# Optimization experiments

Hardware: AMD Instinct MI355X
Metric: run time of the kernel (lower is better)

Reference implementation:

```python
import jax, jax.numpy as jnp
import numpy as np
from jax import lax

COS_BASIS_NO = 24
SCALE = 6.0
SHIFT = 1.0


def make_kern_basis(T_no):
    # [24, T_no] raised-cosine log-time basis, matching the torch loop exactly
    i = jnp.arange(COS_BASIS_NO, dtype=jnp.float32)
    phi = (jnp.pi / 2.0) * i                                  # [24]
    x = jnp.arange(T_no, dtype=jnp.float32)
    raw = SCALE * jnp.log(x + SHIFT + 1e-7)                   # [T_no]
    basis = 0.5 * jnp.cos(raw[None, :] - phi[:, None]) + 0.5  # [24, T_no]
    inside = (raw[None, :] >= phi[:, None] - jnp.pi) & (raw[None, :] <= phi[:, None] + jnp.pi)
    return jnp.where(inside, basis, 0.0)


def causal_grouped_conv(x, kern, sub_no, T_no):
    # x: [B, sub_no, T], kern: [sub_no*hid, T_no] (already flipped like torch)
    # left-pad T_no-1 zeros == the torch zero-padded buffer; cross-correlation
    rhs = kern[:, None, :]  # OIH with I=1 per group
    return lax.conv_general_dilated(
        x, rhs, window_strides=(1,), padding=[(T_no - 1, 0)],
        feature_group_count=sub_no,
        dimension_numbers=("NCH", "OIH", "NCH"))


def setup_inputs() -> dict:
    key = jax.random.key(0)
    ks = jax.random.split(key, 10)
    B, T_data = 8, 5000
    sub_no, E_no, I_no, T_no, hid_no = 20, 2000, 200, 400, 16
    inp = {
        "S_e": jax.random.uniform(ks[0], (B, T_data, E_no), dtype=jnp.float32),
        "S_i": jax.random.uniform(ks[1], (B, T_data, I_no), dtype=jnp.float32),
        "E_scale": jnp.zeros((E_no,), jnp.float32),
        "I_scale": jnp.zeros((I_no,), jnp.float32),
        "W_e_layer1": jax.random.normal(ks[2], (sub_no * hid_no, COS_BASIS_NO), jnp.float32) * 0.01,
        "W_i_layer1": jax.random.normal(ks[3], (sub_no * hid_no, COS_BASIS_NO), jnp.float32) * 0.01,
        "W_layer2": jnp.full((sub_no, hid_no), -1.0, jnp.float32),
        "b_layer1": jnp.zeros((sub_no * hid_no,), jnp.float32),
        "C_syn_e_raw": jax.random.normal(ks[4], (sub_no, E_no), jnp.float32) * 0.01,
        "C_syn_i_raw": jax.random.normal(ks[5], (sub_no, I_no), jnp.float32) * 0.01,
        "V_o": jnp.zeros((1,), jnp.float32),
        "temp": jnp.asarray(1.0, jnp.float32),
        "T_no": T_no,
        "test": 1,
    }
    return inp


def reference(S_e, S_i, E_scale, I_scale, W_e_layer1, W_i_layer1, W_layer2,
              b_layer1, C_syn_e_raw, C_syn_i_raw, V_o, temp, T_no, test):
    sub_no = C_syn_e_raw.shape[0]
    hid_no = W_layer2.shape[1]
    B, T_data, _ = S_e.shape

    if test:
        C_syn_e = jax.nn.softmax(C_syn_e_raw / temp, axis=0)
        C_syn_i = jax.nn.softmax(C_syn_i_raw / temp, axis=0)
    else:
        eps = 1e-8
        ku, kv = jax.random.split(jax.random.key(42))
        u_e = jax.random.uniform(ku, C_syn_e_raw.shape, dtype=C_syn_e_raw.dtype)
        u_i = jax.random.uniform(kv, C_syn_i_raw.shape, dtype=C_syn_i_raw.dtype)
        g_e = -jnp.log(-jnp.log(u_e + eps) + eps)
        g_i = -jnp.log(-jnp.log(u_i + eps) + eps)
        C_syn_e = jax.nn.softmax((C_syn_e_raw + g_e) / temp, axis=0)
        C_syn_i = jax.nn.softmax((C_syn_i_raw + g_i) / temp, axis=0)

    # scale synapses and project onto subunits: [B,T,E] x [E,sub] -> [B,T,sub]
    syn_e = jnp.einsum("bte,se->bts", S_e * jnp.exp(E_scale)[None, None, :], C_syn_e)
    syn_i = jnp.einsum("bti,si->bts", S_i * jnp.exp(I_scale)[None, None, :], C_syn_i)

    kern_basis = make_kern_basis(T_no)                        # [24, T_no]
    ke = jnp.flip(W_e_layer1 @ kern_basis, axis=1)            # [sub*hid, T_no]
    ki = jnp.flip(W_i_layer1 @ kern_basis, axis=1)

    xe = jnp.transpose(syn_e, (0, 2, 1))                      # [B, sub, T]
    xi = jnp.transpose(syn_i, (0, 2, 1))
    conv_e = causal_grouped_conv(xe, ke, sub_no, T_no)        # [B, sub*hid, T]
    conv_i = causal_grouped_conv(xi, ki, sub_no, T_no)
    layer1 = jnp.tanh(conv_e + conv_i + b_layer1[None, :, None])

    # grouped 1x1 conv == per-subunit weighted reduction over hid
    h = layer1.reshape(B, sub_no, hid_no, T_data)
    sub_out = jnp.einsum("bshT,sh->bTs", h, jnp.exp(W_layer2))  # [B, T, sub]
    final = jnp.sum(sub_out, axis=-1) + V_o                    # [B, T]
    return final, sub_out, C_syn_e, C_syn_i
```

## Files before the change

kernel.cpp:

```cpp
#include <hip/hip_runtime.h>
#include <math.h>

#define PI_F 3.14159265358979323846f
#define BSTRIDE 404

__global__ __launch_bounds__(256) void prep_kernel(
    const float* __restrict__ Ce_raw, const float* __restrict__ Ci_raw,
    const float* __restrict__ Escale, const float* __restrict__ Iscale,
    const float* __restrict__ temp,
    float* __restrict__ CsT_e, float* __restrict__ CsT_i,
    float* __restrict__ basis,
    float* __restrict__ outCe, float* __restrict__ outCi)
{
    int id = blockIdx.x * 256 + threadIdx.x;
    if (id < 2000) {
        int e = id;
        float t = temp[0];
        float v[20];
        float m = -1e30f;
        #pragma unroll
        for (int s = 0; s < 20; ++s) { v[s] = Ce_raw[s * 2000 + e] / t; m = fmaxf(m, v[s]); }
        float sum = 0.f;
        #pragma unroll
        for (int s = 0; s < 20; ++s) { v[s] = expf(v[s] - m); sum += v[s]; }
        float inv = 1.f / sum;
        float sc = expf(Escale[e]);
        #pragma unroll
        for (int s = 0; s < 20; ++s) {
            float p = v[s] * inv;
            outCe[s * 2000 + e] = p;
            CsT_e[e * 20 + s] = p * sc;
        }
    } else if (id < 2200) {
        int e = id - 2000;
        float t = temp[0];
        float v[20];
        float m = -1e30f;
        #pragma unroll
        for (int s = 0; s < 20; ++s) { v[s] = Ci_raw[s * 200 + e] / t; m = fmaxf(m, v[s]); }
        float sum = 0.f;
        #pragma unroll
        for (int s = 0; s < 20; ++s) { v[s] = expf(v[s] - m); sum += v[s]; }
        float inv = 1.f / sum;
        float sc = expf(Iscale[e]);
        #pragma unroll
        for (int s = 0; s < 20; ++s) {
            float p = v[s] * inv;
            outCi[s * 200 + e] = p;
            CsT_i[e * 20 + s] = p * sc;
        }
    } else if (id < 2200 + 24 * BSTRIDE) {
        int idx = id - 2200;
        int j = idx / BSTRIDE, d = idx - j * BSTRIDE;
        float val = 0.f;
        if (d < 400) {
            float raw = 6.0f * logf((float)d + 1.0f + 1e-7f);
            float ph = (PI_F * 0.5f) * (float)j;
            if (raw >= ph - PI_F && raw <= ph + PI_F) val = 0.5f * cosf(raw - ph) + 0.5f;
        }
        basis[idx] = val;
    } else if (id < 11896 + 48) {
        int row = 2000 + (id - 11896);
        #pragma unroll
        for (int s = 0; s < 20; ++s) CsT_e[row * 20 + s] = 0.f;
    } else if (id < 11944 + 56) {
        int row = 200 + (id - 11944);
        #pragma unroll
        for (int s = 0; s < 20; ++s) CsT_i[row * 20 + s] = 0.f;
    }
}

template <int NCHUNK>
__global__ __launch_bounds__(256) void syn_kernel(
    const float* __restrict__ S, const float* __restrict__ CsT,
    float* __restrict__ syn, int Eno)
{
    __shared__ float4 tile[64 * 33];
    float* red = reinterpret_cast<float*>(tile);
    const int tid = threadIdx.x;
    const int lane = tid & 63;
    const int w = __builtin_amdgcn_readfirstlane(tid >> 6);
    const int r0 = blockIdx.x * 64;

    float acc[20];
    #pragma unroll
    for (int s = 0; s < 20; ++s) acc[s] = 0.f;

    for (int ch = 0; ch < NCHUNK; ++ch) {
        const int ebase = ch * 128;
        #pragma unroll
        for (int i = 0; i < 8; ++i) {
            int f = tid + i * 256;
            int row = f >> 5, col4 = f & 31;
            int e0 = ebase + col4 * 4;
            float4 v = make_float4(0.f, 0.f, 0.f, 0.f);
            if (e0 + 4 <= Eno)
                v = *reinterpret_cast<const float4*>(S + (size_t)(r0 + row) * Eno + e0);
            tile[row * 33 + col4] = v;
        }
        __syncthreads();

        const float4* crow = reinterpret_cast<const float4*>(CsT + (size_t)(ebase + w * 32) * 20);
        #pragma unroll
        for (int c4 = 0; c4 < 8; ++c4) {
            float4 v = tile[lane * 33 + w * 8 + c4];
            const float4* ct = crow + c4 * 20;
            float vv[4] = {v.x, v.y, v.z, v.w};
            #pragma unroll
            for (int q = 0; q < 4; ++q) {
                float sv = vv[q];
                #pragma unroll
                for (int c5 = 0; c5 < 5; ++c5) {
                    float4 cc = ct[q * 5 + c5];
                    acc[c5 * 4 + 0] = fmaf(sv, cc.x, acc[c5 * 4 + 0]);
                    acc[c5 * 4 + 1] = fmaf(sv, cc.y, acc[c5 * 4 + 1]);
                    acc[c5 * 4 + 2] = fmaf(sv, cc.z, acc[c5 * 4 + 2]);
                    acc[c5 * 4 + 3] = fmaf(sv, cc.w, acc[c5 * 4 + 3]);
                }
            }
        }
        __syncthreads();
    }

    #pragma unroll
    for (int s = 0; s < 20; ++s) red[(w * 64 + lane) * 21 + s] = acc[s];
    __syncthreads();

    #pragma unroll
    for (int i = 0; i < 5; ++i) {
        int p = tid + i * 256;
        int row = p & 63, s = p >> 6;
        float a = red[(0 * 64 + row) * 21 + s] + red[(1 * 64 + row) * 21 + s]
                + red[(2 * 64 + row) * 21 + s] + red[(3 * 64 + row) * 21 + s];
        int r = r0 + row;
        int b = r / 5000, t = r - b * 5000;
        syn[((size_t)b * 20 + s) * 5000 + t] = a;
    }
}

__device__ const int CJ_LO[24] = {0,0,0,0,0,0,0,0,0,4,4,8,12,16,20,28,36,48,64,84,108,140,184,240};
__device__ const int CJ_NB[24] = {1,1,1,1,2,2,3,3,4,4,5,6,7,9,12,15,19,25,31,41,53,65,54,40};

__device__ __forceinline__ int phys4(int g) {
    return (g & ~15) | ((g >> 1) & 7) | ((g & 1) << 3);
}

__global__ __launch_bounds__(128) void conv_kernel(
    const float* __restrict__ syn_e, const float* __restrict__ syn_i,
    const float* __restrict__ basis,
    const float* __restrict__ W_e, const float* __restrict__ W_i,
    const float* __restrict__ b1, const float* __restrict__ W2,
    float* __restrict__ sub_out)
{
    __shared__ float4 win4[16 + 464];
    float4* wbase = win4 + 16;
    float2* win2 = reinterpret_cast<float2*>(wbase);
    const int tid = threadIdx.x;
    const int tile = blockIdx.x, s = blockIdx.y, bz = blockIdx.z;
    const int t0 = tile * 512;

    const float* se = syn_e + ((size_t)bz * 20 + s) * 5000;
    const float* si = syn_i + ((size_t)bz * 20 + s) * 5000;
    for (int l = tid; l < 920; l += 128) {
        int t = t0 - 404 + l;
        float ve = 0.f, vi = 0.f;
        if ((unsigned)t < 5000u) { ve = se[t]; vi = si[t]; }
        int g = l >> 1;
        win2[2 * phys4(g) + (l & 1)] = make_float2(ve, vi);
    }
    __syncthreads();

    float z[16][4];
    #pragma unroll
    for (int h = 0; h < 16; ++h) {
        float bv = b1[s * 16 + h];
        #pragma unroll
        for (int k = 0; k < 4; ++k) z[h][k] = bv;
    }

    const int base = 4 * tid + 400;

    for (int j = 0; j < 24; ++j) {
        const float4* bj4 = reinterpret_cast<const float4*>(basis + j * BSTRIDE);
        const int lo = CJ_LO[j];
        const int nb = CJ_NB[j];
        const int co = lo >> 2;
        float be0 = 0.f, be1 = 0.f, be2 = 0.f, be3 = 0.f;
        float bi0 = 0.f, bi1 = 0.f, bi2 = 0.f, bi3 = 0.f;

        auto body = [&](const float4& V0, const float4& V1,
                        const float4& V2, const float4& V3, const float4& c) {
            be0 = fmaf(c.x, V2.x, be0); bi0 = fmaf(c.x, V2.y, bi0);
            be1 = fmaf(c.x, V2.z, be1); bi1 = fmaf(c.x, V2.w, bi1);
            be2 = fmaf(c.x, V3.x, be2); bi2 = fmaf(c.x, V3.y, bi2);
            be3 = fmaf(c.x, V3.z, be3); bi3 = fmaf(c.x, V3.w, bi3);
            be0 = fmaf(c.y, V1.z, be0); bi0 = fmaf(c.y, V1.w, bi0);
            be1 = fmaf(c.y, V2.x, be1); bi1 = fmaf(c.y, V2.y, bi1);
            be2 = fmaf(c.y, V2.z, be2); bi2 = fmaf(c.y, V2.w, bi2);
            be3 = fmaf(c.y, V3.x, be3); bi3 = fmaf(c.y, V3.y, bi3);
            be0 = fmaf(c.z, V1.x, be0); bi0 = fmaf(c.z, V1.y, bi0);
            be1 = fmaf(c.z, V1.z, be1); bi1 = fmaf(c.z, V1.w, bi1);
            be2 = fmaf(c.z, V2.x, be2); bi2 = fmaf(c.z, V2.y, bi2);
            be3 = fmaf(c.z, V2.z, be3); bi3 = fmaf(c.z, V2.w, bi3);
            be0 = fmaf(c.w, V0.z, be0); bi0 = fmaf(c.w, V0.w, bi0);
            be1 = fmaf(c.w, V1.x, be1); bi1 = fmaf(c.w, V1.y, bi1);
            be2 = fmaf(c.w, V1.z, be2); bi2 = fmaf(c.w, V1.w, bi2);
            be3 = fmaf(c.w, V2.x, be3); bi3 = fmaf(c.w, V2.y, bi3);
        };

        const int g0 = (base - lo) >> 1;
        auto LP = [&](int n, float4& lo4, float4& hi4) {
            int p = phys4(g0 - 2 * n);
            lo4 = wbase[p]; hi4 = wbase[p + 8];
        };

        float4 A0, A1, B0, B1, C0, C1, D0, D1;
        float4 E0, E1, F0, F1, G0, G1, H0, H1;
        LP(-1, A0, A1); LP(0, B0, B1); LP(1, C0, C1); LP(2, D0, D1);
        float4 cB = bj4[co], cC = bj4[co + 1], cD = bj4[co + 2];

        int bb = 0;
        while (bb + 8 <= nb) {
            LP(bb + 3, E0, E1); float4 cE = bj4[co + bb + 3];
            body(B0, B1, A0, A1, cB);
            LP(bb + 4, F0, F1); float4 cF = bj4[co + bb + 4];
            body(C0, C1, B0, B1, cC);
            LP(bb + 5, G0, G1); float4 cG = bj4[co + bb + 5];
            body(D0, D1, C0, C1, cD);
            LP(bb + 6, H0, H1); float4 cH = bj4[co + bb + 6];
            body(E0, E1, D0, D1, cE);
            LP(bb + 7, A0, A1); float4 cI = bj4[co + bb + 7];
            body(F0, F1, E0, E1, cF);
            LP(bb + 8, B0, B1); cB = bj4[co + bb + 8];
            body(G0, G1, F0, F1, cG);
            LP(bb + 9, C0, C1); cC = bj4[co + bb + 9];
            body(H0, H1, G0, G1, cH);
            LP(bb + 10, D0, D1); cD = bj4[co + bb + 10];
            body(A0, A1, H0, H1, cI);
            bb += 8;
        }
        int r = nb - bb;
        if (r > 0) { body(B0, B1, A0, A1, cB);
          if (r > 1) { body(C0, C1, B0, B1, cC);
            if (r > 2) { body(D0, D1, C0, C1, cD);
              if (r > 3) { LP(bb + 3, E0, E1); float4 cE = bj4[co + bb + 3];
                body(E0, E1, D0, D1, cE);
                if (r > 4) { LP(bb + 4, F0, F1); float4 cF = bj4[co + bb + 4];
                  body(F0, F1, E0, E1, cF);
                  if (r > 5) { LP(bb + 5, G0, G1); float4 cG = bj4[co + bb + 5];
                    body(G0, G1, F0, F1, cG);
                    if (r > 6) { LP(bb + 6, H0, H1); float4 cH = bj4[co + bb + 6];
                      body(H0, H1, G0, G1, cH); } } } } } } }

        #pragma unroll
        for (int h = 0; h < 16; ++h) {
            float we = W_e[(s * 16 + h) * 24 + j];
            float wi = W_i[(s * 16 + h) * 24 + j];
            z[h][0] = fmaf(we, be0, fmaf(wi, bi0, z[h][0]));
            z[h][1] = fmaf(we, be1, fmaf(wi, bi1, z[h][1]));
            z[h][2] = fmaf(we, be2, fmaf(wi, bi2, z[h][2]));
            z[h][3] = fmaf(we, be3, fmaf(wi, bi3, z[h][3]));
        }
    }

    float w2v[16];
    #pragma unroll
    for (int h = 0; h < 16; ++h) w2v[h] = __expf(W2[s * 16 + h]);

    #pragma unroll
    for (int k = 0; k < 4; ++k) {
        int t = t0 + 4 * tid + k;
        if (t < 5000) {
            float acc = 0.f;
            #pragma unroll
            for (int h = 0; h < 16; ++h) {
                float e2 = __expf(2.0f * z[h][k]);
                float th = 1.0f - 2.0f / (e2 + 1.0f);
                acc = fmaf(w2v[h], th, acc);
            }
            sub_out[((size_t)bz * 5000 + t) * 20 + s] = acc;
        }
    }
}

__global__ __launch_bounds__(256) void final_kernel(
    const float* __restrict__ sub_out, const float* __restrict__ V_o,
    float* __restrict__ fin)
{
    int r = blockIdx.x * 256 + threadIdx.x;
    if (r < 40000) {
        const float* p = sub_out + (size_t)r * 20;
        float a = V_o[0];
        #pragma unroll
        for (int s = 0; s < 20; ++s) a += p[s];
        fin[r] = a;
    }
}

extern "C" void kernel_launch(void* const* d_in, const int* in_sizes, int n_in,
                              void* d_out, int out_size, void* d_ws, size_t ws_size,
                              hipStream_t stream)
{
    const float* S_e     = (const float*)d_in[0];
    const float* S_i     = (const float*)d_in[1];
    const float* E_scale = (const float*)d_in[2];
    const float* I_scale = (const float*)d_in[3];
    const float* W_e     = (const float*)d_in[4];
    const float* W_i     = (const float*)d_in[5];
    const float* W2      = (const float*)d_in[6];
    const float* b1      = (const float*)d_in[7];
    const float* Ce_raw  = (const float*)d_in[8];
    const float* Ci_raw  = (const float*)d_in[9];
    const float* V_o     = (const float*)d_in[10];
    const float* temp    = (const float*)d_in[11];

    float* out     = (float*)d_out;
    float* fin     = out;
    float* sub_out = out + 40000;
    float* outCe   = out + 840000;
    float* outCi   = out + 880000;

    float* ws    = (float*)d_ws;
    float* CsT_e = ws;
    float* CsT_i = ws + 40960;
    float* basis = ws + 46080;
    float* syn_e = ws + 55776;
    float* syn_i = ws + 855776;

    prep_kernel<<<47, 256, 0, stream>>>(Ce_raw, Ci_raw, E_scale, I_scale, temp,
                                        CsT_e, CsT_i, basis, outCe, outCi);
    syn_kernel<16><<<625, 256, 0, stream>>>(S_e, CsT_e, syn_e, 2000);
    syn_kernel<2><<<625, 256, 0, stream>>>(S_i, CsT_i, syn_i, 200);
    conv_kernel<<<dim3(10, 20, 8), 128, 0, stream>>>(syn_e, syn_i, basis,
                                                     W_e, W_i, b1, W2, sub_out);
    final_kernel<<<157, 256, 0, stream>>>(sub_out, V_o, fin);
}
```

Before: 310.7 us.

## Split syn projection over E into two halves and merge syn kernels

The excitatory projection is split into two K-halves (8 chunks each) run as separate grid slices, and the inhibitory projection joins them in one 3-slice launch. The goal is more blocks in flight across the CUs and one fewer kernel launch. The conv kernel adds the two partial results when it loads its window. The cost is an extra partial buffer in the workspace plus one more global read per conv window element. The S_i slice is much lighter than the others, so the load is uneven across blocks.

```diff
diff --git a/kernel.cpp b/kernel.cpp
--- a/kernel.cpp
+++ b/kernel.cpp
@@ -70,10 +70,11 @@
     }
 }
 
-template <int NCHUNK>
 __global__ __launch_bounds__(256) void syn_kernel(
-    const float* __restrict__ S, const float* __restrict__ CsT,
-    float* __restrict__ syn, int Eno)
+    const float* __restrict__ Se, const float* __restrict__ Si,
+    const float* __restrict__ Ce, const float* __restrict__ Ci,
+    float* __restrict__ outA, float* __restrict__ outB,
+    float* __restrict__ outI)
 {
     __shared__ float4 tile[64 * 33];
     float* red = reinterpret_cast<float*>(tile);
@@ -81,13 +82,21 @@
     const int lane = tid & 63;
     const int w = __builtin_amdgcn_readfirstlane(tid >> 6);
     const int r0 = blockIdx.x * 64;
+    const int z = blockIdx.z;
+
+    const float* S   = (z == 2) ? Si : Se;
+    const float* CsT = (z == 2) ? Ci : Ce;
+    float* out       = (z == 0) ? outA : (z == 1) ? outB : outI;
+    const int Eno    = (z == 2) ? 200 : 2000;
+    const int ch0    = (z == 1) ? 8 : 0;
+    const int nch    = (z == 2) ? 2 : 8;
 
     float acc[20];
     #pragma unroll
     for (int s = 0; s < 20; ++s) acc[s] = 0.f;
 
-    for (int ch = 0; ch < NCHUNK; ++ch) {
-        const int ebase = ch * 128;
+    for (int cc = 0; cc < nch; ++cc) {
+        const int ebase = (ch0 + cc) * 128;
         #pragma unroll
         for (int i = 0; i < 8; ++i) {
             int f = tid + i * 256;
@@ -111,11 +120,11 @@
                 float sv = vv[q];
                 #pragma unroll
                 for (int c5 = 0; c5 < 5; ++c5) {
-                    float4 cc = ct[q * 5 + c5];
-                    acc[c5 * 4 + 0] = fmaf(sv, cc.x, acc[c5 * 4 + 0]);
-                    acc[c5 * 4 + 1] = fmaf(sv, cc.y, acc[c5 * 4 + 1]);
-                    acc[c5 * 4 + 2] = fmaf(sv, cc.z, acc[c5 * 4 + 2]);
-                    acc[c5 * 4 + 3] = fmaf(sv, cc.w, acc[c5 * 4 + 3]);
+                    float4 cc2 = ct[q * 5 + c5];
+                    acc[c5 * 4 + 0] = fmaf(sv, cc2.x, acc[c5 * 4 + 0]);
+                    acc[c5 * 4 + 1] = fmaf(sv, cc2.y, acc[c5 * 4 + 1]);
+                    acc[c5 * 4 + 2] = fmaf(sv, cc2.z, acc[c5 * 4 + 2]);
+                    acc[c5 * 4 + 3] = fmaf(sv, cc2.w, acc[c5 * 4 + 3]);
                 }
             }
         }
@@ -134,7 +143,7 @@
                 + red[(2 * 64 + row) * 21 + s] + red[(3 * 64 + row) * 21 + s];
         int r = r0 + row;
         int b = r / 5000, t = r - b * 5000;
-        syn[((size_t)b * 20 + s) * 5000 + t] = a;
+        out[((size_t)b * 20 + s) * 5000 + t] = a;
     }
 }
 
@@ -146,8 +155,8 @@
 }
 
 __global__ __launch_bounds__(128) void conv_kernel(
-    const float* __restrict__ syn_e, const float* __restrict__ syn_i,
-    const float* __restrict__ basis,
+    const float* __restrict__ syn_eA, const float* __restrict__ syn_eB,
+    const float* __restrict__ syn_i, const float* __restrict__ basis,
     const float* __restrict__ W_e, const float* __restrict__ W_i,
     const float* __restrict__ b1, const float* __restrict__ W2,
     float* __restrict__ sub_out)
@@ -159,12 +168,13 @@
     const int tile = blockIdx.x, s = blockIdx.y, bz = blockIdx.z;
     const int t0 = tile * 512;
 
-    const float* se = syn_e + ((size_t)bz * 20 + s) * 5000;
-    const float* si = syn_i + ((size_t)bz * 20 + s) * 5000;
+    const float* seA = syn_eA + ((size_t)bz * 20 + s) * 5000;
+    const float* seB = syn_eB + ((size_t)bz * 20 + s) * 5000;
+    const float* si  = syn_i  + ((size_t)bz * 20 + s) * 5000;
     for (int l = tid; l < 920; l += 128) {
         int t = t0 - 404 + l;
         float ve = 0.f, vi = 0.f;
-        if ((unsigned)t < 5000u) { ve = se[t]; vi = si[t]; }
+        if ((unsigned)t < 5000u) { ve = seA[t] + seB[t]; vi = si[t]; }
         int g = l >> 1;
         win2[2 * phys4(g) + (l & 1)] = make_float2(ve, vi);
     }
@@ -320,18 +330,19 @@
     float* outCe   = out + 840000;
     float* outCi   = out + 880000;
 
-    float* ws    = (float*)d_ws;
-    float* CsT_e = ws;
-    float* CsT_i = ws + 40960;
-    float* basis = ws + 46080;
-    float* syn_e = ws + 55776;
-    float* syn_i = ws + 855776;
+    float* ws     = (float*)d_ws;
+    float* CsT_e  = ws;
+    float* CsT_i  = ws + 40960;
+    float* basis  = ws + 46080;
+    float* syn_eA = ws + 55776;
+    float* syn_eB = ws + 855776;
+    float* syn_i  = ws + 1655776;
 
     prep_kernel<<<47, 256, 0, stream>>>(Ce_raw, Ci_raw, E_scale, I_scale, temp,
                                         CsT_e, CsT_i, basis, outCe, outCi);
-    syn_kernel<16><<<625, 256, 0, stream>>>(S_e, CsT_e, syn_e, 2000);
-    syn_kernel<2><<<625, 256, 0, stream>>>(S_i, CsT_i, syn_i, 200);
-    conv_kernel<<<dim3(10, 20, 8), 128, 0, stream>>>(syn_e, syn_i, basis,
+    syn_kernel<<<dim3(625, 1, 3), 256, 0, stream>>>(S_e, S_i, CsT_e, CsT_i,
+                                                    syn_eA, syn_eB, syn_i);
+    conv_kernel<<<dim3(10, 20, 8), 128, 0, stream>>>(syn_eA, syn_eB, syn_i, basis,
                                                      W_e, W_i, b1, W2, sub_out);
     final_kernel<<<157, 256, 0, stream>>>(sub_out, V_o, fin);
 }
```

Result: faster. 300.9 us (-3.2%).
